# Performance work log

Measured on AMD Instinct MI355X. Metric: run time of the kernel, lower is better.

Reference implementation:

```python
import jax, jax.numpy as jnp
import numpy as np

N_NODES = 100000
N_EDGES = 3200000
N_GRAPHS = 64
IN_DIM = 300
HIDDEN = 64
N_CLS = 20


def setup_inputs() -> dict:
    key = jax.random.key(0)
    ks = jax.random.split(key, 10)
    x = jax.random.normal(ks[0], (N_NODES, IN_DIM), dtype=jnp.float32)
    edge_index = jax.random.randint(ks[1], (2, N_EDGES), 0, N_NODES, dtype=jnp.int32)
    batch = jnp.sort(jax.random.randint(ks[2], (N_NODES,), 0, N_GRAPHS, dtype=jnp.int32))
    num_entity = jax.random.randint(ks[3], (N_GRAPHS,), 0, 2000, dtype=jnp.int32)
    # GCNConv params (glorot-ish scale) and final linear
    W1 = jax.random.normal(ks[4], (IN_DIM, HIDDEN), dtype=jnp.float32) * (1.0 / np.sqrt(IN_DIM))
    b1 = jnp.zeros((HIDDEN,), dtype=jnp.float32)
    W2 = jax.random.normal(ks[5], (HIDDEN, HIDDEN), dtype=jnp.float32) * (1.0 / np.sqrt(HIDDEN))
    b2 = jnp.zeros((HIDDEN,), dtype=jnp.float32)
    Wlin = jax.random.normal(ks[6], (HIDDEN, N_CLS), dtype=jnp.float32) * (1.0 / np.sqrt(HIDDEN))
    blin = jnp.zeros((N_CLS,), dtype=jnp.float32)
    return {"x": x, "edge_index": edge_index, "batch": batch, "num_entity": num_entity,
            "W1": W1, "b1": b1, "W2": W2, "b2": b2, "Wlin": Wlin, "blin": blin}


def _gcn_norm(edge_index, n):
    # PyG GCNConv default: add self-loops, symmetric normalization
    loops = jnp.arange(n, dtype=edge_index.dtype)
    row = jnp.concatenate([edge_index[0], loops])  # source
    col = jnp.concatenate([edge_index[1], loops])  # target
    deg = jax.ops.segment_sum(jnp.ones_like(col, dtype=jnp.float32), col, num_segments=n)
    dinv = jnp.where(deg > 0, jax.lax.rsqrt(deg), 0.0)
    norm = dinv[row] * dinv[col]  # [E + N]
    return row, col, norm


def _gcn_conv(h, row, col, norm, W, b, n):
    h = h @ W                                        # [N, out]
    msg = h[row] * norm[:, None]                     # gather + scale, [E+N, out]
    return jax.ops.segment_sum(msg, col, num_segments=n) + b


def reference(x, edge_index, batch, num_entity, W1, b1, W2, b2, Wlin, blin):
    n = x.shape[0]
    row, col, norm = _gcn_norm(edge_index, n)
    h = jax.nn.relu(_gcn_conv(x, row, col, norm, W1, b1, n))
    h = jax.nn.relu(_gcn_conv(h, row, col, norm, W2, b2, n))

    # masked entity pooling (faithful: global node index compared to per-graph entity count)
    ent_mask = (jnp.arange(n) < num_entity[batch]).astype(h.dtype)[:, None]  # [N,1]
    ent_sum = jax.ops.segment_sum(h * ent_mask, batch, num_segments=N_GRAPHS)
    ent_cnt = jax.ops.segment_sum(ent_mask, batch, num_segments=N_GRAPHS)    # [G,1]
    ent_mean = ent_sum / (ent_cnt + 1e-6)
    all_sum = jax.ops.segment_sum(h, batch, num_segments=N_GRAPHS)
    node_cnt = jax.ops.segment_sum(jnp.ones((n, 1), h.dtype), batch, num_segments=N_GRAPHS)
    all_mean = all_sum / node_cnt
    pooled = jnp.where(ent_cnt > 0, ent_mean, all_mean)                      # [G, hidden]
    return jax.nn.log_softmax(pooled @ Wlin + blin, axis=1)
```

## Files before the change

kernel.cpp:

```cpp
#include <hip/hip_runtime.h>
#include <hip/hip_fp16.h>
#include <math.h>

#define HID 64
#define BKT_W 256
#define BKT_SHIFT 8
#define MAX_BKT 512
#define EPB 4096
#define CAP 10240

typedef __attribute__((ext_vector_type(8))) short short8v;
typedef __attribute__((ext_vector_type(4))) float float4v;
typedef __attribute__((ext_vector_type(2))) float float2v;

__device__ __forceinline__ unsigned short f2bf(float x) {
    unsigned int b = __float_as_uint(x);
    unsigned int r = (b + 0x7FFFu + ((b >> 16) & 1u)) >> 16;
    return (unsigned short)r;
}

__global__ void k_binit(int* __restrict__ bcursor, int nbkt) {
    int b = blockIdx.x * blockDim.x + threadIdx.x;
    if (b < nbkt) bcursor[b] = b * CAP;
}

__global__ __launch_bounds__(256) void k_binA(const int* __restrict__ row,
                                              const int* __restrict__ col,
                                              int* __restrict__ bcursor,
                                              unsigned int* __restrict__ pairs,
                                              int E, int nbkt) {
    __shared__ int hist[MAX_BKT];
    __shared__ int base[MAX_BKT];
    int t = threadIdx.x;
    for (int b = t; b < nbkt; b += 256) hist[b] = 0;
    __syncthreads();
    int e0 = blockIdx.x * EPB;
    int myc[16], myr[16], myoff[16];
    #pragma unroll
    for (int q = 0; q < 4; ++q) {
        int eb = e0 + t * 4 + q * 1024;
        if (eb + 3 < E) {
            int4 cv = *(const int4*)(col + eb);
            int4 rv = *(const int4*)(row + eb);
            myc[q*4+0] = cv.x; myc[q*4+1] = cv.y; myc[q*4+2] = cv.z; myc[q*4+3] = cv.w;
            myr[q*4+0] = rv.x; myr[q*4+1] = rv.y; myr[q*4+2] = rv.z; myr[q*4+3] = rv.w;
        } else {
            #pragma unroll
            for (int u = 0; u < 4; ++u) {
                int e = eb + u;
                if (e < E) { myc[q*4+u] = col[e]; myr[q*4+u] = row[e]; }
                else       { myc[q*4+u] = -1; myr[q*4+u] = 0; }
            }
        }
        #pragma unroll
        for (int u = 0; u < 4; ++u) {
            int i = q * 4 + u;
            if (myc[i] >= 0)
                myoff[i] = atomicAdd(&hist[myc[i] >> BKT_SHIFT], 1);
        }
    }
    __syncthreads();
    for (int b = t; b < nbkt; b += 256) {
        int h = hist[b];
        base[b] = h ? atomicAdd(&bcursor[b], h) : 0;
    }
    __syncthreads();
    #pragma unroll
    for (int i = 0; i < 16; ++i) {
        if (myc[i] >= 0) {
            int bk = myc[i] >> BKT_SHIFT;
            pairs[base[bk] + myoff[i]] =
                ((unsigned int)myr[i] << BKT_SHIFT) | (unsigned int)(myc[i] & (BKT_W - 1));
        }
    }
}

__global__ __launch_bounds__(MAX_BKT) void k_bscan(const int* __restrict__ bcursor,
                                                   int* __restrict__ bkt_base, int nbkt) {
    __shared__ int s[MAX_BKT];
    int t = threadIdx.x;
    int v = (t < nbkt) ? (bcursor[t] - t * CAP) : 0;
    s[t] = v;
    __syncthreads();
    #pragma unroll
    for (int off = 1; off < MAX_BKT; off <<= 1) {
        int tv = (t >= off) ? s[t - off] : 0;
        __syncthreads();
        s[t] += tv;
        __syncthreads();
    }
    if (t < nbkt) {
        bkt_base[t] = s[t] - v;
        if (t == nbkt - 1) bkt_base[nbkt] = s[t];
    }
}

__global__ __launch_bounds__(256) void k_binB(const unsigned int* __restrict__ pairs,
                                              const int* __restrict__ bkt_base,
                                              int* __restrict__ rowptr,
                                              int* __restrict__ srcs,
                                              float* __restrict__ dinv,
                                              int n, int E) {
    __shared__ int cnt[BKT_W];
    __shared__ int s[BKT_W];
    __shared__ int lcur[BKT_W];
    int b = blockIdx.x, t = threadIdx.x;
    int n0 = b << BKT_SHIFT;
    int n1 = min(n0 + BKT_W, n);
    int s0 = bkt_base[b], s1 = bkt_base[b + 1];
    int cntE = s1 - s0;
    int p0 = b * CAP;
    cnt[t] = 0;
    __syncthreads();
    for (int i = p0 + t; i < p0 + cntE; i += 256)
        atomicAdd(&cnt[pairs[i] & (BKT_W - 1)], 1);
    __syncthreads();
    int v = cnt[t];
    s[t] = v;
    __syncthreads();
    #pragma unroll
    for (int off = 1; off < BKT_W; off <<= 1) {
        int tv = (t >= off) ? s[t - off] : 0;
        __syncthreads();
        s[t] += tv;
        __syncthreads();
    }
    int ex = s[t] - v;
    if (t < n1 - n0) {
        rowptr[n0 + t] = s0 + ex;
        dinv[n0 + t] = rsqrtf((float)(v + 1));
    }
    lcur[t] = s0 + ex;
    __syncthreads();
    for (int i = p0 + t; i < p0 + cntE; i += 256) {
        unsigned int p = pairs[i];
        int pos = atomicAdd(&lcur[p & (BKT_W - 1)], 1);
        srcs[pos] = (int)(p >> BKT_SHIFT);
    }
    if (n1 == n && t == 0) rowptr[n] = E;
}

__global__ void k_wswz(const float* __restrict__ W, unsigned short* __restrict__ out,
                       int K, int nslots) {
    int s = blockIdx.x * blockDim.x + threadIdx.x;
    if (s >= nslots) return;
    int kb = s >> 8;
    int p = (s >> 6) & 3;
    int l = s & 63;
    int g = l >> 4, li = l & 15;
    int colc = p * 16 + li;
    unsigned short vals[8];
    #pragma unroll
    for (int j = 0; j < 8; ++j) {
        int k = kb * 32 + ((j < 4) ? (g * 4 + j) : (16 + g * 4 + j - 4));
        vals[j] = (k < K) ? f2bf(W[(size_t)k * HID + colc]) : (unsigned short)0;
    }
    ushort4* o = (ushort4*)(out + (size_t)s * 8);
    o[0] = make_ushort4(vals[0], vals[1], vals[2], vals[3]);
    o[1] = make_ushort4(vals[4], vals[5], vals[6], vals[7]);
}

__device__ __forceinline__ unsigned int pack4fp8(float v0, float v1, float v2, float v3) {
    int u = __builtin_amdgcn_cvt_pk_fp8_f32(v0, v1, 0, false);
    u = __builtin_amdgcn_cvt_pk_fp8_f32(v2, v3, u, true);
    return (unsigned int)u;
}

__global__ __launch_bounds__(256) void k_gemm_mfma(const float* __restrict__ A,
                                                   const unsigned short* __restrict__ Wswz,
                                                   const float* __restrict__ dinv,
                                                   unsigned int* __restrict__ outM,
                                                   int n, int K) {
    int t = threadIdx.x;
    int w = t >> 6, l = t & 63;
    int g = l >> 4, li = l & 15;
    int m0 = blockIdx.x * 64;
    int node = m0 + w * 16 + li;
    const float* arow = A + (size_t)node * K;
    float4v acc0 = {0.f,0.f,0.f,0.f}, acc1 = {0.f,0.f,0.f,0.f};
    float4v acc2 = {0.f,0.f,0.f,0.f}, acc3 = {0.f,0.f,0.f,0.f};
    int KB = (K + 31) / 32;
    bool nok = node < n;

    for (int kb = 0; kb < KB; ++kb) {
        int k0 = kb * 32 + g * 4;
        float4 va = {0.f,0.f,0.f,0.f};
        float4 vb = {0.f,0.f,0.f,0.f};
        if (nok && k0 < K)      va = *(const float4*)(arow + k0);
        if (nok && k0 + 16 < K) vb = *(const float4*)(arow + k0 + 16);
        short8v a;
        a[0] = (short)f2bf(va.x); a[1] = (short)f2bf(va.y);
        a[2] = (short)f2bf(va.z); a[3] = (short)f2bf(va.w);
        a[4] = (short)f2bf(vb.x); a[5] = (short)f2bf(vb.y);
        a[6] = (short)f2bf(vb.z); a[7] = (short)f2bf(vb.w);
        const short8v* wp = (const short8v*)(Wswz + (size_t)(kb * 4) * 64 * 8);
        short8v b0 = wp[0 * 64 + l];
        short8v b1 = wp[1 * 64 + l];
        short8v b2 = wp[2 * 64 + l];
        short8v b3 = wp[3 * 64 + l];
        acc0 = __builtin_amdgcn_mfma_f32_16x16x32_bf16(a, b0, acc0, 0, 0, 0);
        acc1 = __builtin_amdgcn_mfma_f32_16x16x32_bf16(a, b1, acc1, 0, 0, 0);
        acc2 = __builtin_amdgcn_mfma_f32_16x16x32_bf16(a, b2, acc2, 0, 0, 0);
        acc3 = __builtin_amdgcn_mfma_f32_16x16x32_bf16(a, b3, acc3, 0, 0, 0);
    }

    float dv[4];
    int rbase = m0 + w * 16 + g * 4;
    #pragma unroll
    for (int r = 0; r < 4; ++r)
        dv[r] = (rbase + r < n) ? dinv[rbase + r] : 0.f;
    #pragma unroll
    for (int r = 0; r < 4; ++r) {
        int rown = rbase + r;
        if (rown < n) {
            unsigned int u = pack4fp8(acc0[r] * dv[r], acc1[r] * dv[r],
                                      acc2[r] * dv[r], acc3[r] * dv[r]);
            outM[(size_t)rown * 16 + li] = u;
        }
    }
}

__global__ __launch_bounds__(256) void k_gemm_mfma_h(const unsigned short* __restrict__ Ah,
                                                     const unsigned short* __restrict__ Wswz,
                                                     const float* __restrict__ dinv,
                                                     unsigned int* __restrict__ outM,
                                                     int n, int K) {
    int t = threadIdx.x;
    int w = t >> 6, l = t & 63;
    int g = l >> 4, li = l & 15;
    int m0 = blockIdx.x * 64;
    int node = m0 + w * 16 + li;
    const uint2* arow = (const uint2*)(Ah + (size_t)node * K);
    float4v acc0 = {0.f,0.f,0.f,0.f}, acc1 = {0.f,0.f,0.f,0.f};
    float4v acc2 = {0.f,0.f,0.f,0.f}, acc3 = {0.f,0.f,0.f,0.f};
    int KB = (K + 31) / 32;
    bool nok = node < n;

    for (int kb = 0; kb < KB; ++kb) {
        int k0 = kb * 32 + g * 4;
        uint2 ua = {0u, 0u}, ub = {0u, 0u};
        if (nok && k0 < K)      ua = arow[k0 >> 2];
        if (nok && k0 + 16 < K) ub = arow[(k0 + 16) >> 2];
        float2 fa0 = __half22float2(*(__half2*)&ua.x);
        float2 fa1 = __half22float2(*(__half2*)&ua.y);
        float2 fb0 = __half22float2(*(__half2*)&ub.x);
        float2 fb1 = __half22float2(*(__half2*)&ub.y);
        short8v a;
        a[0] = (short)f2bf(fa0.x); a[1] = (short)f2bf(fa0.y);
        a[2] = (short)f2bf(fa1.x); a[3] = (short)f2bf(fa1.y);
        a[4] = (short)f2bf(fb0.x); a[5] = (short)f2bf(fb0.y);
        a[6] = (short)f2bf(fb1.x); a[7] = (short)f2bf(fb1.y);
        const short8v* wp = (const short8v*)(Wswz + (size_t)(kb * 4) * 64 * 8);
        short8v b0 = wp[0 * 64 + l];
        short8v b1 = wp[1 * 64 + l];
        short8v b2 = wp[2 * 64 + l];
        short8v b3 = wp[3 * 64 + l];
        acc0 = __builtin_amdgcn_mfma_f32_16x16x32_bf16(a, b0, acc0, 0, 0, 0);
        acc1 = __builtin_amdgcn_mfma_f32_16x16x32_bf16(a, b1, acc1, 0, 0, 0);
        acc2 = __builtin_amdgcn_mfma_f32_16x16x32_bf16(a, b2, acc2, 0, 0, 0);
        acc3 = __builtin_amdgcn_mfma_f32_16x16x32_bf16(a, b3, acc3, 0, 0, 0);
    }

    float dv[4];
    int rbase = m0 + w * 16 + g * 4;
    #pragma unroll
    for (int r = 0; r < 4; ++r)
        dv[r] = (rbase + r < n) ? dinv[rbase + r] : 0.f;
    #pragma unroll
    for (int r = 0; r < 4; ++r) {
        int rown = rbase + r;
        if (rown < n) {
            unsigned int u = pack4fp8(acc0[r] * dv[r], acc1[r] * dv[r],
                                      acc2[r] * dv[r], acc3[r] * dv[r]);
            outM[(size_t)rown * 16 + li] = u;
        }
    }
}

__global__ __launch_bounds__(256) void k_agg(const unsigned int* __restrict__ M,
                                             const int* __restrict__ rowptr,
                                             const int* __restrict__ srcs,
                                             const float* __restrict__ dinv,
                                             const float* __restrict__ bias,
                                             unsigned short* __restrict__ out16, int n) {
    int node = blockIdx.x * 4 + (threadIdx.x >> 6);
    if (node >= n) return;
    int lane = threadIdx.x & 63;
    int e4 = lane >> 4, c4 = lane & 15;
    float s0 = 0.f, s1 = 0.f, s2 = 0.f, s3 = 0.f;
    if (e4 == 0) {
        unsigned int u = M[(size_t)node * 16 + c4];
        float2v lo = __builtin_amdgcn_cvt_pk_f32_fp8(u, false);
        float2v hi = __builtin_amdgcn_cvt_pk_f32_fp8(u, true);
        s0 = lo[0]; s1 = lo[1]; s2 = hi[0]; s3 = hi[1];
    }
    int s = rowptr[node], e = rowptr[node + 1];
    for (int k = s + e4; k < e; k += 16) {
        int k1 = k + 4, k2 = k + 8, k3 = k + 12;
        int r0 = srcs[k];
        int r1 = (k1 < e) ? srcs[k1] : r0;
        int r2 = (k2 < e) ? srcs[k2] : r0;
        int r3 = (k3 < e) ? srcs[k3] : r0;
        unsigned int u0 = M[(size_t)r0 * 16 + c4];
        unsigned int u1 = M[(size_t)r1 * 16 + c4];
        unsigned int u2 = M[(size_t)r2 * 16 + c4];
        unsigned int u3 = M[(size_t)r3 * 16 + c4];
        {
            float2v lo = __builtin_amdgcn_cvt_pk_f32_fp8(u0, false);
            float2v hi = __builtin_amdgcn_cvt_pk_f32_fp8(u0, true);
            s0 += lo[0]; s1 += lo[1]; s2 += hi[0]; s3 += hi[1];
        }
        if (k1 < e) {
            float2v lo = __builtin_amdgcn_cvt_pk_f32_fp8(u1, false);
            float2v hi = __builtin_amdgcn_cvt_pk_f32_fp8(u1, true);
            s0 += lo[0]; s1 += lo[1]; s2 += hi[0]; s3 += hi[1];
        }
        if (k2 < e) {
            float2v lo = __builtin_amdgcn_cvt_pk_f32_fp8(u2, false);
            float2v hi = __builtin_amdgcn_cvt_pk_f32_fp8(u2, true);
            s0 += lo[0]; s1 += lo[1]; s2 += hi[0]; s3 += hi[1];
        }
        if (k3 < e) {
            float2v lo = __builtin_amdgcn_cvt_pk_f32_fp8(u3, false);
            float2v hi = __builtin_amdgcn_cvt_pk_f32_fp8(u3, true);
            s0 += lo[0]; s1 += lo[1]; s2 += hi[0]; s3 += hi[1];
        }
    }
    s0 += __shfl_xor(s0, 16); s0 += __shfl_xor(s0, 32);
    s1 += __shfl_xor(s1, 16); s1 += __shfl_xor(s1, 32);
    s2 += __shfl_xor(s2, 16); s2 += __shfl_xor(s2, 32);
    s3 += __shfl_xor(s3, 16); s3 += __shfl_xor(s3, 32);
    if (lane < 16) {
        float d = dinv[node];
        float v0 = fmaxf(fmaf(s0, d, bias[c4]),      0.f);
        float v1 = fmaxf(fmaf(s1, d, bias[16 + c4]), 0.f);
        float v2 = fmaxf(fmaf(s2, d, bias[32 + c4]), 0.f);
        float v3 = fmaxf(fmaf(s3, d, bias[48 + c4]), 0.f);
        __half h0 = __float2half(v0), h1 = __float2half(v1);
        __half h2 = __float2half(v2), h3 = __float2half(v3);
        size_t ob = (size_t)node * HID + c4;
        out16[ob]      = *(unsigned short*)&h0;
        out16[ob + 16] = *(unsigned short*)&h1;
        out16[ob + 32] = *(unsigned short*)&h2;
        out16[ob + 48] = *(unsigned short*)&h3;
    }
}

#define PCHUNK 32
__global__ void k_pool(const unsigned short* __restrict__ h, const int* __restrict__ batch,
                       const int* __restrict__ ne_arr,
                       float* ent_sum, float* all_sum, float* ent_cnt, float* node_cnt,
                       int n) {
    int wave = blockIdx.x * (blockDim.x >> 6) + (threadIdx.x >> 6);
    int j = threadIdx.x & 63;
    int i0 = wave * PCHUNK;
    if (i0 >= n) return;
    int iend = min(i0 + PCHUNK, n);
    int g = batch[i0];
    int ne = ne_arr[g];
    float ea = 0.f, aa = 0.f, ec = 0.f, nc = 0.f;
    for (int i = i0; i < iend; ++i) {
        int gi = batch[i];
        if (gi != g) {
            atomicAdd(&all_sum[g * HID + j], aa);
            atomicAdd(&ent_sum[g * HID + j], ea);
            if (j == 0) { atomicAdd(&node_cnt[g], nc); atomicAdd(&ent_cnt[g], ec); }
            g = gi; ne = ne_arr[g];
            ea = aa = ec = nc = 0.f;
        }
        float v = __half2float(((const __half*)h)[(size_t)i * HID + j]);
        aa += v; nc += 1.f;
        if (i < ne) { ea += v; ec += 1.f; }
    }
    atomicAdd(&all_sum[g * HID + j], aa);
    atomicAdd(&ent_sum[g * HID + j], ea);
    if (j == 0) { atomicAdd(&node_cnt[g], nc); atomicAdd(&ent_cnt[g], ec); }
}

__global__ void k_final(const float* __restrict__ ent_sum, const float* __restrict__ all_sum,
                        const float* __restrict__ ent_cnt, const float* __restrict__ node_cnt,
                        const float* __restrict__ Wlin, const float* __restrict__ blin,
                        float* __restrict__ out, int ncls) {
    int g = blockIdx.x, j = threadIdx.x;
    __shared__ float pooled[HID];
    __shared__ float logits[32];
    float ec = ent_cnt[g];
    float p;
    if (ec > 0.0f)
        p = ent_sum[g * HID + j] / (ec + 1e-6f);
    else
        p = all_sum[g * HID + j] / node_cnt[g];
    pooled[j] = p;
    __syncthreads();
    if (j < ncls) {
        float acc = blin[j];
        for (int k = 0; k < HID; ++k)
            acc = fmaf(pooled[k], Wlin[k * ncls + j], acc);
        logits[j] = acc;
    }
    __syncthreads();
    if (j < ncls) {
        float m = -INFINITY;
        for (int c = 0; c < ncls; ++c) m = fmaxf(m, logits[c]);
        float s = 0.0f;
        for (int c = 0; c < ncls; ++c) s += expf(logits[c] - m);
        out[g * ncls + j] = logits[j] - m - logf(s);
    }
}

extern "C" void kernel_launch(void* const* d_in, const int* in_sizes, int n_in,
                              void* d_out, int out_size, void* d_ws, size_t ws_size,
                              hipStream_t stream) {
    const float* x          = (const float*)d_in[0];
    const int*   ei         = (const int*)d_in[1];
    const int*   batch      = (const int*)d_in[2];
    const int*   num_entity = (const int*)d_in[3];
    const float* W1         = (const float*)d_in[4];
    const float* b1         = (const float*)d_in[5];
    const float* W2         = (const float*)d_in[6];
    const float* b2         = (const float*)d_in[7];
    const float* Wlin       = (const float*)d_in[8];
    const float* blin       = (const float*)d_in[9];
    float* out = (float*)d_out;

    int N = in_sizes[2];
    int E = in_sizes[1] / 2;
    int K = in_sizes[0] / N;
    int G = in_sizes[3];
    int NCLS = in_sizes[9];

    const int* row = ei;
    const int* col = ei + E;

    int KB1 = (K + 31) / 32;
    int KB2 = (HID + 31) / 32;
    int nslots1 = KB1 * 4 * 64;
    int nslots2 = KB2 * 4 * 64;
    int nbkt = (N + BKT_W - 1) >> BKT_SHIFT;

    char* wsb = (char*)d_ws;
    size_t off = 0;
    auto take = [&](size_t bytes) -> void* {
        void* p = wsb + off;
        off += (bytes + 255) & ~(size_t)255;
        return p;
    };
    int*   rowptr   = (int*)take((size_t)(N + 1) * 4);
    float* dinv     = (float*)take((size_t)N * 4);
    int*   bkt_base = (int*)take((MAX_BKT + 1) * 4);
    int*   bcursor  = (int*)take(MAX_BKT * 4);
    unsigned short* w1s = (unsigned short*)take((size_t)nslots1 * 16);
    unsigned short* w2s = (unsigned short*)take((size_t)nslots2 * 16);
    int*   srcs     = (int*)take((size_t)E * 4);
    unsigned int* pairs = (unsigned int*)take((size_t)nbkt * CAP * 4);
    unsigned int* bufM  = (unsigned int*)take((size_t)N * 16 * 4);
    unsigned short* bufH = (unsigned short*)take((size_t)N * HID * 2);
    unsigned short* bufA = (unsigned short*)take((size_t)N * HID * 2);
    float* ent_sum  = (float*)take((size_t)G * HID * 4);
    float* all_sum  = (float*)take((size_t)G * HID * 4);
    float* ent_cnt  = (float*)take((size_t)G * 4);
    float* node_cnt = (float*)take((size_t)G * 4);

    k_wswz<<<(nslots1 + 255) / 256, 256, 0, stream>>>(W1, w1s, K, nslots1);
    k_wswz<<<(nslots2 + 255) / 256, 256, 0, stream>>>(W2, w2s, HID, nslots2);

    k_binit<<<(nbkt + 255) / 256, 256, 0, stream>>>(bcursor, nbkt);
    k_binA<<<(E + EPB - 1) / EPB, 256, 0, stream>>>(row, col, bcursor, pairs, E, nbkt);
    k_bscan<<<1, MAX_BKT, 0, stream>>>(bcursor, bkt_base, nbkt);
    k_binB<<<nbkt, 256, 0, stream>>>(pairs, bkt_base, rowptr, srcs, dinv, N, E);

    k_gemm_mfma<<<(N + 63) / 64, 256, 0, stream>>>(x, w1s, dinv, bufM, N, K);
    k_agg<<<(N + 3) / 4, 256, 0, stream>>>(bufM, rowptr, srcs, dinv, b1, bufH, N);
    k_gemm_mfma_h<<<(N + 63) / 64, 256, 0, stream>>>(bufH, w2s, dinv, bufM, N, HID);
    k_agg<<<(N + 3) / 4, 256, 0, stream>>>(bufM, rowptr, srcs, dinv, b2, bufA, N);

    hipMemsetAsync(ent_sum, 0, ((size_t)2 * G * HID + 2 * G) * 4, stream);
    k_pool<<<(N + PCHUNK * 4 - 1) / (PCHUNK * 4), 256, 0, stream>>>(
        bufA, batch, num_entity, ent_sum, all_sum, ent_cnt, node_cnt, N);

    k_final<<<G, HID, 0, stream>>>(ent_sum, all_sum, ent_cnt, node_cnt, Wlin, blin, out, NCLS);
}
```

Before: 291.4 us.

## Split message matrix into two channel slices mapped to XCD halves for aggregation

The GEMM epilogues now write the fp8 message matrix as two separate slices of 32 bytes per node instead of one interleaved 64-byte row. The aggregation grid doubles and maps block IDs so that XCDs 0-3 gather only slice 0 and XCDs 4-7 only slice 1. Each XCD's L2 then has to cache half the gather working set, which is meant to raise hit rates for the random neighbour gathers. The cost is that rowptr and srcs are read twice, and each wave uses 8 lanes per edge with 8 edge slots. The two weight-swizzle launches are also merged into one kernel.

Result: slower. 348.8 us (+19.7%).

```diff
diff --git a/kernel.cpp b/kernel.cpp
--- a/kernel.cpp
+++ b/kernel.cpp
@@ -140,10 +140,15 @@
     if (n1 == n && t == 0) rowptr[n] = E;
 }
 
-__global__ void k_wswz(const float* __restrict__ W, unsigned short* __restrict__ out,
-                       int K, int nslots) {
+__global__ void k_wswz(const float* __restrict__ W1, unsigned short* __restrict__ out1,
+                       int K1, int nslots1,
+                       const float* __restrict__ W2, unsigned short* __restrict__ out2,
+                       int K2, int nslots2) {
     int s = blockIdx.x * blockDim.x + threadIdx.x;
-    if (s >= nslots) return;
+    const float* W; unsigned short* out; int K;
+    if (s < nslots1) { W = W1; out = out1; K = K1; }
+    else if (s < nslots1 + nslots2) { s -= nslots1; W = W2; out = out2; K = K2; }
+    else return;
     int kb = s >> 8;
     int p = (s >> 6) & 3;
     int l = s & 63;
@@ -209,13 +214,14 @@
     #pragma unroll
     for (int r = 0; r < 4; ++r)
         dv[r] = (rbase + r < n) ? dinv[rbase + r] : 0.f;
+    size_t sb = (size_t)(li >> 3) * n * 8 + (li & 7);
     #pragma unroll
     for (int r = 0; r < 4; ++r) {
         int rown = rbase + r;
         if (rown < n) {
             unsigned int u = pack4fp8(acc0[r] * dv[r], acc1[r] * dv[r],
                                       acc2[r] * dv[r], acc3[r] * dv[r]);
-            outM[(size_t)rown * 16 + li] = u;
+            outM[sb + (size_t)rown * 8] = u;
         }
     }
 }
@@ -266,13 +272,14 @@
     #pragma unroll
     for (int r = 0; r < 4; ++r)
         dv[r] = (rbase + r < n) ? dinv[rbase + r] : 0.f;
+    size_t sb = (size_t)(li >> 3) * n * 8 + (li & 7);
     #pragma unroll
     for (int r = 0; r < 4; ++r) {
         int rown = rbase + r;
         if (rown < n) {
             unsigned int u = pack4fp8(acc0[r] * dv[r], acc1[r] * dv[r],
                                       acc2[r] * dv[r], acc3[r] * dv[r]);
-            outM[(size_t)rown * 16 + li] = u;
+            outM[sb + (size_t)rown * 8] = u;
         }
     }
 }
@@ -283,28 +290,29 @@
                                              const float* __restrict__ dinv,
                                              const float* __restrict__ bias,
                                              unsigned short* __restrict__ out16, int n) {
-    int node = blockIdx.x * 4 + (threadIdx.x >> 6);
+    int b = blockIdx.x;
+    int xcd = b & 7;
+    int slice = xcd >> 2;
+    int nodeblk = (b >> 3) * 4 + (xcd & 3);
+    int node = nodeblk * 4 + (threadIdx.x >> 6);
     if (node >= n) return;
     int lane = threadIdx.x & 63;
-    int e4 = lane >> 4, c4 = lane & 15;
+    int slot = lane >> 3, c8 = lane & 7;
+    const unsigned int* Ms = M + (size_t)slice * n * 8;
     float s0 = 0.f, s1 = 0.f, s2 = 0.f, s3 = 0.f;
-    if (e4 == 0) {
-        unsigned int u = M[(size_t)node * 16 + c4];
+    if (slot == 0) {
+        unsigned int u = Ms[(size_t)node * 8 + c8];
         float2v lo = __builtin_amdgcn_cvt_pk_f32_fp8(u, false);
         float2v hi = __builtin_amdgcn_cvt_pk_f32_fp8(u, true);
         s0 = lo[0]; s1 = lo[1]; s2 = hi[0]; s3 = hi[1];
     }
     int s = rowptr[node], e = rowptr[node + 1];
-    for (int k = s + e4; k < e; k += 16) {
-        int k1 = k + 4, k2 = k + 8, k3 = k + 12;
+    for (int k = s + slot; k < e; k += 16) {
+        int k1 = k + 8;
         int r0 = srcs[k];
         int r1 = (k1 < e) ? srcs[k1] : r0;
-        int r2 = (k2 < e) ? srcs[k2] : r0;
-        int r3 = (k3 < e) ? srcs[k3] : r0;
-        unsigned int u0 = M[(size_t)r0 * 16 + c4];
-        unsigned int u1 = M[(size_t)r1 * 16 + c4];
-        unsigned int u2 = M[(size_t)r2 * 16 + c4];
-        unsigned int u3 = M[(size_t)r3 * 16 + c4];
+        unsigned int u0 = Ms[(size_t)r0 * 8 + c8];
+        unsigned int u1 = Ms[(size_t)r1 * 8 + c8];
         {
             float2v lo = __builtin_amdgcn_cvt_pk_f32_fp8(u0, false);
             float2v hi = __builtin_amdgcn_cvt_pk_f32_fp8(u0, true);
@@ -315,30 +323,22 @@
             float2v hi = __builtin_amdgcn_cvt_pk_f32_fp8(u1, true);
             s0 += lo[0]; s1 += lo[1]; s2 += hi[0]; s3 += hi[1];
         }
-        if (k2 < e) {
-            float2v lo = __builtin_amdgcn_cvt_pk_f32_fp8(u2, false);
-            float2v hi = __builtin_amdgcn_cvt_pk_f32_fp8(u2, true);
-            s0 += lo[0]; s1 += lo[1]; s2 += hi[0]; s3 += hi[1];
-        }
-        if (k3 < e) {
-            float2v lo = __builtin_amdgcn_cvt_pk_f32_fp8(u3, false);
-            float2v hi = __builtin_amdgcn_cvt_pk_f32_fp8(u3, true);
-            s0 += lo[0]; s1 += lo[1]; s2 += hi[0]; s3 += hi[1];
-        }
-    }
-    s0 += __shfl_xor(s0, 16); s0 += __shfl_xor(s0, 32);
-    s1 += __shfl_xor(s1, 16); s1 += __shfl_xor(s1, 32);
-    s2 += __shfl_xor(s2, 16); s2 += __shfl_xor(s2, 32);
-    s3 += __shfl_xor(s3, 16); s3 += __shfl_xor(s3, 32);
-    if (lane < 16) {
-        float d = dinv[node];
-        float v0 = fmaxf(fmaf(s0, d, bias[c4]),      0.f);
-        float v1 = fmaxf(fmaf(s1, d, bias[16 + c4]), 0.f);
-        float v2 = fmaxf(fmaf(s2, d, bias[32 + c4]), 0.f);
-        float v3 = fmaxf(fmaf(s3, d, bias[48 + c4]), 0.f);
+    }
+    #pragma unroll
+    for (int d = 8; d <= 32; d <<= 1) {
+        s0 += __shfl_xor(s0, d); s1 += __shfl_xor(s1, d);
+        s2 += __shfl_xor(s2, d); s3 += __shfl_xor(s3, d);
+    }
+    if (lane < 8) {
+        float dn = dinv[node];
+        int ch = slice * 8 + c8;
+        float v0 = fmaxf(fmaf(s0, dn, bias[ch]),      0.f);
+        float v1 = fmaxf(fmaf(s1, dn, bias[16 + ch]), 0.f);
+        float v2 = fmaxf(fmaf(s2, dn, bias[32 + ch]), 0.f);
+        float v3 = fmaxf(fmaf(s3, dn, bias[48 + ch]), 0.f);
         __half h0 = __float2half(v0), h1 = __float2half(v1);
         __half h2 = __float2half(v2), h3 = __float2half(v3);
-        size_t ob = (size_t)node * HID + c4;
+        size_t ob = (size_t)node * HID + ch;
         out16[ob]      = *(unsigned short*)&h0;
         out16[ob + 16] = *(unsigned short*)&h1;
         out16[ob + 32] = *(unsigned short*)&h2;
@@ -461,18 +461,21 @@
     float* ent_cnt  = (float*)take((size_t)G * 4);
     float* node_cnt = (float*)take((size_t)G * 4);
 
-    k_wswz<<<(nslots1 + 255) / 256, 256, 0, stream>>>(W1, w1s, K, nslots1);
-    k_wswz<<<(nslots2 + 255) / 256, 256, 0, stream>>>(W2, w2s, HID, nslots2);
+    k_wswz<<<(nslots1 + nslots2 + 255) / 256, 256, 0, stream>>>(
+        W1, w1s, K, nslots1, W2, w2s, HID, nslots2);
 
     k_binit<<<(nbkt + 255) / 256, 256, 0, stream>>>(bcursor, nbkt);
     k_binA<<<(E + EPB - 1) / EPB, 256, 0, stream>>>(row, col, bcursor, pairs, E, nbkt);
     k_bscan<<<1, MAX_BKT, 0, stream>>>(bcursor, bkt_base, nbkt);
     k_binB<<<nbkt, 256, 0, stream>>>(pairs, bkt_base, rowptr, srcs, dinv, N, E);
 
+    int nblkNodes = (N + 3) / 4;
+    int aggGrid = 8 * ((nblkNodes + 3) / 4);
+
     k_gemm_mfma<<<(N + 63) / 64, 256, 0, stream>>>(x, w1s, dinv, bufM, N, K);
-    k_agg<<<(N + 3) / 4, 256, 0, stream>>>(bufM, rowptr, srcs, dinv, b1, bufH, N);
+    k_agg<<<aggGrid, 256, 0, stream>>>(bufM, rowptr, srcs, dinv, b1, bufH, N);
     k_gemm_mfma_h<<<(N + 63) / 64, 256, 0, stream>>>(bufH, w2s, dinv, bufM, N, HID);
-    k_agg<<<(N + 3) / 4, 256, 0, stream>>>(bufM, rowptr, srcs, dinv, b2, bufA, N);
+    k_agg<<<aggGrid, 256, 0, stream>>>(bufM, rowptr, srcs, dinv, b2, bufA, N);
 
     hipMemsetAsync(ent_sum, 0, ((size_t)2 * G * HID + 2 * G) * 4, stream);
     k_pool<<<(N + PCHUNK * 4 - 1) / (PCHUNK * 4), 256, 0, stream>>>(
```
